# Kernel tuning notes

Measured on AMD Instinct MI355X. Metric: run time of the kernel, lower is better.

## Reference

```python
import jax, jax.numpy as jnp
import numpy as np

OUT_F, IN_F, RANK = 4096, 4096, 32
N_TOK = 8192  # batch 4 * seq 2048, flattened


def setup_inputs() -> dict:
    key = jax.random.key(0)
    k_x, k_w, k_s, k_a, k_b, k_bias = jax.random.split(key, 6)
    x = jax.random.normal(k_x, (N_TOK, IN_F), dtype=jnp.float32)
    # ternary weights in {-1, 0, +1}, stored as int8 buffer
    weight_q = (jax.random.randint(k_w, (OUT_F, IN_F), 0, 3) - 1).astype(jnp.int8)
    # per-output-channel absmean scale, shape [out, 1], positive
    scale = 0.02 + 0.05 * jax.random.uniform(k_s, (OUT_F, 1), dtype=jnp.float32)
    lora_A = 0.01 * jax.random.normal(k_a, (OUT_F, RANK), dtype=jnp.float32)
    lora_B = 0.01 * jax.random.normal(k_b, (RANK, IN_F), dtype=jnp.float32)
    bias = 0.01 * jax.random.normal(k_bias, (OUT_F,), dtype=jnp.float32)
    return {"x": x, "weight_q": weight_q, "scale": scale,
            "lora_A": lora_A, "lora_B": lora_B, "bias": bias}


def reference(x, weight_q, scale, lora_A, lora_B, bias):
    # out = (x @ W_q^T) * scale_per_out_channel + x @ B^T @ A^T + bias
    Wq = weight_q.astype(x.dtype)                       # dequantize {-1,0,1}
    out = jnp.einsum('ti,oi->to', x, Wq) * scale.reshape(1, -1)
    # low-rank LoRA residual: (x @ B^T) @ A^T, rank-RANK bottleneck
    out = out + (x @ lora_B.T) @ lora_A.T
    out = out + bias
    return out
```

## Files before the change

### kernel.cpp

```cpp
#include <hip/hip_runtime.h>
#include <stdint.h>

typedef unsigned short u16;
typedef __attribute__((ext_vector_type(8))) __bf16 bf16x8;
typedef __attribute__((ext_vector_type(4))) float f32x4;

__device__ __forceinline__ u16 f2bf(float f) {
  unsigned int u = __builtin_bit_cast(unsigned int, f);
  u = (u + 0x7FFFu + ((u >> 16) & 1u)) >> 16;
  return (u16)u;
}
__device__ __forceinline__ u16 tern2bf(int s) {
  return s == 0 ? (u16)0 : (s > 0 ? (u16)0x3F80 : (u16)0xBF80);
}

#define GLOAD_LDS16(g, l)                                                          \
  __builtin_amdgcn_global_load_lds((__attribute__((address_space(1))) void*)(g),   \
                                   (__attribute__((address_space(3))) void*)(l),   \
                                   16, 0, 0)

#define M_TOK 8192
#define N_OUT 4096
#define K_IN  4096
#define RANK  32

#define WS_XB    0ull
#define WS_WB    67108864ull
#define WS_BB    100663296ull
#define WS_A32   100925440ull
#define WS_T32   101187584ull
#define WS_TPART 101711872ull
#define WS_FLAG  110100480ull

__global__ void k_convert_x(const float4* __restrict__ x, ushort4* __restrict__ xb, int n4) {
  int stride = gridDim.x * blockDim.x;
  for (int i = blockIdx.x * blockDim.x + threadIdx.x; i < n4; i += stride) {
    float4 v = x[i];
    ushort4 o;
    o.x = f2bf(v.x); o.y = f2bf(v.y); o.z = f2bf(v.z); o.w = f2bf(v.w);
    xb[i] = o;
  }
}

__global__ void k_detect_wtype(const int* __restrict__ w, int* __restrict__ flag) {
  int v = w[threadIdx.x];
  bool ok = (v >= -1 && v <= 1);
  unsigned long long m = __ballot(ok);
  if (threadIdx.x == 0) *flag = (m == ~0ull) ? 1 : 0;
}

__global__ void k_convert_w(const void* __restrict__ wq, const int* __restrict__ flag,
                            ushort4* __restrict__ wb, int n4) {
  int is32 = *flag;
  int stride = gridDim.x * blockDim.x;
  for (int i = blockIdx.x * blockDim.x + threadIdx.x; i < n4; i += stride) {
    int s0, s1, s2, s3;
    if (is32) {
      int4 c = ((const int4*)wq)[i];
      s0 = c.x; s1 = c.y; s2 = c.z; s3 = c.w;
    } else {
      char4 c = ((const char4*)wq)[i];
      s0 = c.x; s1 = c.y; s2 = c.z; s3 = c.w;
    }
    ushort4 o;
    o.x = tern2bf(s0); o.y = tern2bf(s1); o.z = tern2bf(s2); o.w = tern2bf(s3);
    wb[i] = o;
  }
}

__global__ void k_prep_B(const float* __restrict__ loraB, u16* __restrict__ bb) {
  int idx = blockIdx.x * blockDim.x + threadIdx.x;
  if (idx < RANK * K_IN) bb[idx] = f2bf(loraB[idx]);
}

__global__ void k_prep_A(const float* __restrict__ loraA, const float* __restrict__ scale,
                         u16* __restrict__ a32) {
  int idx = blockIdx.x * blockDim.x + threadIdx.x;
  if (idx >= N_OUT * RANK) return;
  int o = idx >> 5;
  a32[idx] = f2bf(loraA[idx] / scale[o]);
}

__global__ __launch_bounds__(256) void k_lora_T(const u16* __restrict__ xb,
                                                const u16* __restrict__ bb,
                                                float* __restrict__ tpart) {
  __shared__ u16 As[64 * 32];
  __shared__ u16 Bs[32 * 32];
  int mt = blockIdx.x >> 3;
  int ks = blockIdx.x & 7;
  int tid = threadIdx.x, lane = tid & 63, wv = tid >> 6;
  int m0 = mt * 64;
  int kbase0 = ks * 512;
  f32x4 acc[2] = {};
  for (int step = 0; step < 16; ++step) {
    int kb = kbase0 + step * 32;
    __syncthreads();
    {
      const u16* src = xb + (size_t)(m0 + (tid >> 2)) * K_IN + kb + (tid & 3) * 8;
      GLOAD_LDS16(src, &As[tid * 8]);
    }
    if (tid < 128) {
      const u16* src = bb + (size_t)(tid >> 2) * K_IN + kb + (tid & 3) * 8;
      GLOAD_LDS16(src, &Bs[tid * 8]);
    }
    __syncthreads();
    bf16x8 a = *(const bf16x8*)&As[(wv * 16 + (lane & 15)) * 32 + (lane >> 4) * 8];
#pragma unroll
    for (int ni = 0; ni < 2; ++ni) {
      bf16x8 b = *(const bf16x8*)&Bs[(ni * 16 + (lane & 15)) * 32 + (lane >> 4) * 8];
      acc[ni] = __builtin_amdgcn_mfma_f32_16x16x32_bf16(a, b, acc[ni], 0, 0, 0);
    }
  }
#pragma unroll
  for (int ni = 0; ni < 2; ++ni)
#pragma unroll
    for (int r = 0; r < 4; ++r) {
      int row = m0 + wv * 16 + (lane >> 4) * 4 + r;
      int col = ni * 16 + (lane & 15);
      tpart[((size_t)ks * M_TOK + row) * RANK + col] = acc[ni][r];
    }
}

__global__ void k_reduce_T(const float* __restrict__ tpart, u16* __restrict__ t32) {
  int idx = blockIdx.x * blockDim.x + threadIdx.x;
  if (idx >= M_TOK * RANK) return;
  int t = idx >> 5, r = idx & 31;
  float v = 0.f;
#pragma unroll
  for (int s = 0; s < 8; ++s) v += tpart[((size_t)s * M_TOK + t) * RANK + r];
  t32[idx] = f2bf(v);
}

__global__ __launch_bounds__(1024, 4) void k_gemm8(const u16* __restrict__ xb,
                                                   const u16* __restrict__ wb,
                                                   const u16* __restrict__ t32,
                                                   const u16* __restrict__ a32,
                                                   const float* __restrict__ scale,
                                                   const float* __restrict__ bias,
                                                   float* __restrict__ out) {
  __shared__ u16 As[4][8192];
  __shared__ u16 Bs[4][8192];
  const int tid = threadIdx.x;
  const int l = tid & 63, w = tid >> 6;
  const int wm = w >> 2, wn = w & 3;
  const int bid = blockIdx.x;
  const int swz = (bid & 7) * 64 + (bid >> 3);
  const int m0 = (swz >> 4) * 256, n0 = (swz & 15) * 256;

  const int srow = tid >> 2;
  const int scx = ((tid & 3) ^ ((tid >> 3) & 3)) * 8;
  const int ldst = tid * 8;
  const int r15 = l & 15;
  const int cxr = (((l >> 4) ^ ((r15 >> 1) & 3)) * 8);

  f32x4 acc[4][4] = {};

  u16* AsF = &As[0][0];
  u16* BsF = &Bs[0][0];
  const u16* axs = xb + (size_t)(m0 + srow) * K_IN + scx;
  const u16* bxs = wb + (size_t)(n0 + srow) * K_IN + scx;

#pragma unroll
  for (int ts = 0; ts < 3; ++ts) {
    GLOAD_LDS16(axs + ts * 32, AsF + ts * 8192 + ldst);
    GLOAD_LDS16(bxs + ts * 32, BsF + ts * 8192 + ldst);
  }
  asm volatile("s_waitcnt vmcnt(4)" ::: "memory");
  asm volatile("s_barrier" ::: "memory");

  const int abase = (wm * 64 + r15) * 32 + cxr;
  const int bbase = (wn * 64 + r15) * 32 + cxr;

  const u16* ap = axs + 96;
  const u16* bp = bxs + 96;

  bf16x8 fa[4], fb[4];

#define SA(DST) { GLOAD_LDS16(ap, AsF + (DST) * 8192 + ldst); ap += 32; }
#define SB(DST) { GLOAD_LDS16(bp, BsF + (DST) * 8192 + ldst); bp += 32; }
#define W2  asm volatile("s_waitcnt vmcnt(2)" ::: "memory");
#define W0  asm volatile("s_waitcnt vmcnt(0)" ::: "memory");
#define BARR asm volatile("s_barrier" ::: "memory");
#define READN(NS)                                                                   \
  { const u16* An = AsF + (NS) * 8192;                                              \
    const u16* Bn = BsF + (NS) * 8192;                                              \
    _Pragma("unroll") for (int mi = 0; mi < 4; ++mi)                                \
        fa[mi] = *(const bf16x8*)&An[abase + mi * 512];                             \
    _Pragma("unroll") for (int nj = 0; nj < 4; ++nj)                                \
        fb[nj] = *(const bf16x8*)&Bn[bbase + nj * 512]; }

#define TILE(STAGE, WAIT, RD, BAR)                                                  \
  {                                                                                 \
    STAGE                                                                           \
    __builtin_amdgcn_s_setprio(1);                                                  \
    _Pragma("unroll") for (int mi = 0; mi < 4; ++mi)                                \
    _Pragma("unroll") for (int nj = 0; nj < 4; ++nj)                                \
        acc[mi][nj] =                                                               \
            __builtin_amdgcn_mfma_f32_16x16x32_bf16(fa[mi], fb[nj], acc[mi][nj], 0, 0, 0); \
    __builtin_amdgcn_s_setprio(0);                                                  \
    WAIT                                                                            \
    RD                                                                              \
    BAR                                                                             \
  }

  READN(0)

#pragma unroll 1
  for (int t = 0; t < 124; t += 4) {
    TILE(SA(3) SB(3), W2, READN(1), BARR)
    TILE(SA(0) SB(0), W2, READN(2), BARR)
    TILE(SA(1) SB(1), W2, READN(3), BARR)
    TILE(SA(2) SB(2), W2, READN(0), BARR)
  }
  TILE(SA(3) SB(3), W2, READN(1), BARR)
  {
    const u16* la = t32 + (size_t)(m0 + srow) * RANK + scx;
    const u16* lb = a32 + (size_t)(n0 + srow) * RANK + scx;
    TILE({ GLOAD_LDS16(la, AsF + 0 * 8192 + ldst); GLOAD_LDS16(lb, BsF + 0 * 8192 + ldst); },
         W2, READN(2), BARR)
  }
  TILE(, W0, READN(3), BARR)
  TILE(, , READN(0), BARR)
  TILE(, , , )

#pragma unroll
  for (int nj = 0; nj < 4; ++nj) {
    int col = n0 + wn * 64 + nj * 16 + r15;
    float s = scale[col], bv = bias[col];
#pragma unroll
    for (int mi = 0; mi < 4; ++mi) {
      int row = m0 + wm * 64 + mi * 16 + (l >> 4) * 4;
#pragma unroll
      for (int r = 0; r < 4; ++r)
        out[(size_t)(row + r) * N_OUT + col] = acc[mi][nj][r] * s + bv;
    }
  }
}

extern "C" void kernel_launch(void* const* d_in, const int* in_sizes, int n_in,
                              void* d_out, int out_size, void* d_ws, size_t ws_size,
                              hipStream_t stream) {
  const float* x     = (const float*)d_in[0];
  const void*  wq    = d_in[1];
  const float* scale = (const float*)d_in[2];
  const float* loraA = (const float*)d_in[3];
  const float* loraB = (const float*)d_in[4];
  const float* bias  = (const float*)d_in[5];
  float* out = (float*)d_out;

  char* ws = (char*)d_ws;
  u16*   xb    = (u16*)(ws + WS_XB);
  u16*   wbuf  = (u16*)(ws + WS_WB);
  u16*   bb    = (u16*)(ws + WS_BB);
  u16*   a32   = (u16*)(ws + WS_A32);
  u16*   t32   = (u16*)(ws + WS_T32);
  float* tpart = (float*)(ws + WS_TPART);
  int*   flag  = (int*)(ws + WS_FLAG);

  k_convert_x<<<2048, 256, 0, stream>>>((const float4*)x, (ushort4*)xb, M_TOK * K_IN / 4);
  k_detect_wtype<<<1, 64, 0, stream>>>((const int*)wq, flag);
  k_prep_B<<<512, 256, 0, stream>>>(loraB, bb);
  k_prep_A<<<512, 256, 0, stream>>>(loraA, scale, a32);
  k_convert_w<<<2048, 256, 0, stream>>>(wq, flag, (ushort4*)wbuf, N_OUT * K_IN / 4);
  k_lora_T<<<1024, 256, 0, stream>>>(xb, bb, tpart);
  k_reduce_T<<<1024, 256, 0, stream>>>(tpart, t32);
  k_gemm8<<<512, 1024, 0, stream>>>(xb, wbuf, t32, a32, scale, bias, out);

  (void)in_sizes; (void)n_in; (void)out_size; (void)ws_size;
}
```

Measured before the change: 315.5 us.

## Keep ternary weights as int8 in GEMM and expand to bf16 in registers

```diff
diff --git a/kernel.cpp b/kernel.cpp
--- a/kernel.cpp
+++ b/kernel.cpp
@@ -10,8 +10,17 @@
   u = (u + 0x7FFFu + ((u >> 16) & 1u)) >> 16;
   return (u16)u;
 }
-__device__ __forceinline__ u16 tern2bf(int s) {
-  return s == 0 ? (u16)0 : (s > 0 ? (u16)0x3F80 : (u16)0xBF80);
+__device__ __forceinline__ bf16x8 expand8(unsigned q0, unsigned q1) {
+  unsigned x = (q0 & 0xFFu) | ((q0 & 0xFF00u) << 8);
+  unsigned y = ((q0 >> 16) & 0xFFu) | ((q0 >> 8) & 0xFF0000u);
+  unsigned z = (q1 & 0xFFu) | ((q1 & 0xFF00u) << 8);
+  unsigned w = ((q1 >> 16) & 0xFFu) | ((q1 >> 8) & 0xFF0000u);
+  uint4 o;
+  o.x = ((x & 0x10001u) * 0x3F80u) | ((x & 0x800080u) << 8);
+  o.y = ((y & 0x10001u) * 0x3F80u) | ((y & 0x800080u) << 8);
+  o.z = ((z & 0x10001u) * 0x3F80u) | ((z & 0x800080u) << 8);
+  o.w = ((w & 0x10001u) * 0x3F80u) | ((w & 0x800080u) << 8);
+  return __builtin_bit_cast(bf16x8, o);
 }
 
 #define GLOAD_LDS16(g, l)                                                          \
@@ -49,22 +58,29 @@
   if (threadIdx.x == 0) *flag = (m == ~0ull) ? 1 : 0;
 }
 
-__global__ void k_convert_w(const void* __restrict__ wq, const int* __restrict__ flag,
-                            ushort4* __restrict__ wb, int n4) {
+__global__ void k_convert_w8(const void* __restrict__ wq, const int* __restrict__ flag,
+                             char* __restrict__ wb8) {
   int is32 = *flag;
   int stride = gridDim.x * blockDim.x;
-  for (int i = blockIdx.x * blockDim.x + threadIdx.x; i < n4; i += stride) {
-    int s0, s1, s2, s3;
+  int total = N_OUT * K_IN / 8;
+  for (int i = blockIdx.x * blockDim.x + threadIdx.x; i < total; i += stride) {
+    int row = i >> 9;
+    int jb = (i & 511) * 8;
+    uint2 pk;
     if (is32) {
-      int4 c = ((const int4*)wq)[i];
-      s0 = c.x; s1 = c.y; s2 = c.z; s3 = c.w;
+      const int* s = (const int*)wq + (size_t)row * K_IN + jb;
+      unsigned lo = 0, hi = 0;
+#pragma unroll
+      for (int k2 = 0; k2 < 4; ++k2) lo |= ((unsigned)s[k2] & 0xFFu) << (8 * k2);
+#pragma unroll
+      for (int k2 = 0; k2 < 4; ++k2) hi |= ((unsigned)s[4 + k2] & 0xFFu) << (8 * k2);
+      pk.x = lo; pk.y = hi;
     } else {
-      char4 c = ((const char4*)wq)[i];
-      s0 = c.x; s1 = c.y; s2 = c.z; s3 = c.w;
-    }
-    ushort4 o;
-    o.x = tern2bf(s0); o.y = tern2bf(s1); o.z = tern2bf(s2); o.w = tern2bf(s3);
-    wb[i] = o;
+      pk = *(const uint2*)((const char*)wq + (size_t)row * K_IN + jb);
+    }
+    int jin = jb & 63, g = jb >> 6;
+    int p = ((jin >> 3) & 3) * 16 + (jin >> 5) * 8;
+    *(uint2*)(wb8 + (size_t)row * K_IN + (g << 6) + p) = pk;
   }
 }
 
@@ -132,14 +148,14 @@
 }
 
 __global__ __launch_bounds__(1024, 4) void k_gemm8(const u16* __restrict__ xb,
-                                                   const u16* __restrict__ wb,
+                                                   const char* __restrict__ wb8,
                                                    const u16* __restrict__ t32,
                                                    const u16* __restrict__ a32,
                                                    const float* __restrict__ scale,
                                                    const float* __restrict__ bias,
                                                    float* __restrict__ out) {
   __shared__ u16 As[4][8192];
-  __shared__ u16 Bs[4][8192];
+  __shared__ char Bs8[4][16384];
   const int tid = threadIdx.x;
   const int l = tid & 63, w = tid >> 6;
   const int wm = w >> 2, wn = w & 3;
@@ -152,44 +168,64 @@
   const int ldst = tid * 8;
   const int r15 = l & 15;
   const int cxr = (((l >> 4) ^ ((r15 >> 1) & 3)) * 8);
+  const int cxB = (((l >> 4) ^ ((r15 >> 1) & 3)) * 16);
 
   f32x4 acc[4][4] = {};
 
   u16* AsF = &As[0][0];
-  u16* BsF = &Bs[0][0];
+  char* Bs8F = &Bs8[0][0];
   const u16* axs = xb + (size_t)(m0 + srow) * K_IN + scx;
-  const u16* bxs = wb + (size_t)(n0 + srow) * K_IN + scx;
-
-#pragma unroll
-  for (int ts = 0; ts < 3; ++ts) {
-    GLOAD_LDS16(axs + ts * 32, AsF + ts * 8192 + ldst);
-    GLOAD_LDS16(bxs + ts * 32, BsF + ts * 8192 + ldst);
-  }
-  asm volatile("s_waitcnt vmcnt(4)" ::: "memory");
+  const char* bsrc = wb8 + (size_t)(n0 + (tid >> 2)) * 4096 +
+                     (size_t)(((tid & 3) ^ ((tid >> 3) & 3)) * 16);
+
+  GLOAD_LDS16(bsrc, Bs8F + 0 * 16384 + tid * 16); bsrc += 64;
+  GLOAD_LDS16(bsrc, Bs8F + 1 * 16384 + tid * 16); bsrc += 64;
+#pragma unroll
+  for (int ts = 0; ts < 3; ++ts) GLOAD_LDS16(axs + ts * 32, AsF + ts * 8192 + ldst);
+  asm volatile("s_waitcnt vmcnt(1)" ::: "memory");
   asm volatile("s_barrier" ::: "memory");
 
   const int abase = (wm * 64 + r15) * 32 + cxr;
-  const int bbase = (wn * 64 + r15) * 32 + cxr;
+  const int bb8base = (wn * 64 + r15) * 64 + cxB;
+  const int lbbase = (wn * 64 + r15) * 32 + cxr;
 
   const u16* ap = axs + 96;
-  const u16* bp = bxs + 96;
 
   bf16x8 fa[4], fb[4];
+  uint2 stash[4];
 
 #define SA(DST) { GLOAD_LDS16(ap, AsF + (DST) * 8192 + ldst); ap += 32; }
-#define SB(DST) { GLOAD_LDS16(bp, BsF + (DST) * 8192 + ldst); bp += 32; }
+#define SBP(DST) { GLOAD_LDS16(bsrc, Bs8F + (DST) * 16384 + tid * 16); bsrc += 64; }
+#define SLB { GLOAD_LDS16(a32 + (size_t)(n0 + srow) * RANK + scx, Bs8F + 16384 + ldst * 2); }
+#define SAL { GLOAD_LDS16(t32 + (size_t)(m0 + srow) * RANK + scx, AsF + 0 * 8192 + ldst); }
 #define W2  asm volatile("s_waitcnt vmcnt(2)" ::: "memory");
+#define W1  asm volatile("s_waitcnt vmcnt(1)" ::: "memory");
 #define W0  asm volatile("s_waitcnt vmcnt(0)" ::: "memory");
 #define BARR asm volatile("s_barrier" ::: "memory");
-#define READN(NS)                                                                   \
+#define RDE(NS, BS)                                                                 \
   { const u16* An = AsF + (NS) * 8192;                                              \
-    const u16* Bn = BsF + (NS) * 8192;                                              \
+    _Pragma("unroll") for (int mi = 0; mi < 4; ++mi)                                \
+        fa[mi] = *(const bf16x8*)&An[abase + mi * 512];                             \
+    const char* Bn = Bs8F + (BS) * 16384;                                           \
+    _Pragma("unroll") for (int nj = 0; nj < 4; ++nj) {                              \
+      uint4 r_ = *(const uint4*)&Bn[bb8base + nj * 1024];                           \
+      fb[nj] = expand8(r_.x, r_.y);                                                 \
+      stash[nj] = make_uint2(r_.z, r_.w); } }
+#define RDO(NS)                                                                     \
+  { const u16* An = AsF + (NS) * 8192;                                              \
     _Pragma("unroll") for (int mi = 0; mi < 4; ++mi)                                \
         fa[mi] = *(const bf16x8*)&An[abase + mi * 512];                             \
     _Pragma("unroll") for (int nj = 0; nj < 4; ++nj)                                \
-        fb[nj] = *(const bf16x8*)&Bn[bbase + nj * 512]; }
-
-#define TILE(STAGE, WAIT, RD, BAR)                                                  \
+        fb[nj] = expand8(stash[nj].x, stash[nj].y); }
+#define RDL                                                                         \
+  { const u16* An = AsF;                                                            \
+    _Pragma("unroll") for (int mi = 0; mi < 4; ++mi)                                \
+        fa[mi] = *(const bf16x8*)&An[abase + mi * 512];                             \
+    const u16* Ln = (const u16*)(Bs8F + 16384);                                     \
+    _Pragma("unroll") for (int nj = 0; nj < 4; ++nj)                                \
+        fb[nj] = *(const bf16x8*)&Ln[lbbase + nj * 512]; }
+
+#define TILE(STAGE, WAIT, RD)                                                       \
   {                                                                                 \
     STAGE                                                                           \
     __builtin_amdgcn_s_setprio(1);                                                  \
@@ -200,28 +236,31 @@
     __builtin_amdgcn_s_setprio(0);                                                  \
     WAIT                                                                            \
     RD                                                                              \
-    BAR                                                                             \
-  }
-
-  READN(0)
+    BARR                                                                            \
+  }
+
+  RDE(0, 0)
 
 #pragma unroll 1
-  for (int t = 0; t < 124; t += 4) {
-    TILE(SA(3) SB(3), W2, READN(1), BARR)
-    TILE(SA(0) SB(0), W2, READN(2), BARR)
-    TILE(SA(1) SB(1), W2, READN(3), BARR)
-    TILE(SA(2) SB(2), W2, READN(0), BARR)
-  }
-  TILE(SA(3) SB(3), W2, READN(1), BARR)
-  {
-    const u16* la = t32 + (size_t)(m0 + srow) * RANK + scx;
-    const u16* lb = a32 + (size_t)(n0 + srow) * RANK + scx;
-    TILE({ GLOAD_LDS16(la, AsF + 0 * 8192 + ldst); GLOAD_LDS16(lb, BsF + 0 * 8192 + ldst); },
-         W2, READN(2), BARR)
-  }
-  TILE(, W0, READN(3), BARR)
-  TILE(, , READN(0), BARR)
-  TILE(, , , )
+  for (int it = 0; it < 15; ++it) {
+    TILE(SA(3) SBP(2), W2, RDO(1))
+    TILE(SA(0),        W1, RDE(2, 1))
+    TILE(SA(1) SBP(3), W2, RDO(3))
+    TILE(SA(2),        W1, RDE(0, 2))
+    TILE(SA(3) SBP(0), W2, RDO(1))
+    TILE(SA(0),        W1, RDE(2, 3))
+    TILE(SA(1) SBP(1), W2, RDO(3))
+    TILE(SA(2),        W1, RDE(0, 0))
+  }
+  TILE(SA(3) SBP(2), W2, RDO(1))
+  TILE(SA(0),        W1, RDE(2, 1))
+  TILE(SA(1) SBP(3), W2, RDO(3))
+  TILE(SA(2),        W1, RDE(0, 2))
+  TILE(SA(3) SLB,    W2, RDO(1))
+  TILE(SAL,          W2, RDE(2, 3))
+  TILE(,             W0, RDO(3))
+  TILE(,             ,   RDL)
+  TILE(,             ,   )
 
 #pragma unroll
   for (int nj = 0; nj < 4; ++nj) {
@@ -250,7 +289,7 @@
 
   char* ws = (char*)d_ws;
   u16*   xb    = (u16*)(ws + WS_XB);
-  u16*   wbuf  = (u16*)(ws + WS_WB);
+  char*  wb8   = (char*)(ws + WS_WB);
   u16*   bb    = (u16*)(ws + WS_BB);
   u16*   a32   = (u16*)(ws + WS_A32);
   u16*   t32   = (u16*)(ws + WS_T32);
@@ -261,10 +300,10 @@
   k_detect_wtype<<<1, 64, 0, stream>>>((const int*)wq, flag);
   k_prep_B<<<512, 256, 0, stream>>>(loraB, bb);
   k_prep_A<<<512, 256, 0, stream>>>(loraA, scale, a32);
-  k_convert_w<<<2048, 256, 0, stream>>>(wq, flag, (ushort4*)wbuf, N_OUT * K_IN / 4);
+  k_convert_w8<<<2048, 256, 0, stream>>>(wq, flag, wb8);
   k_lora_T<<<1024, 256, 0, stream>>>(xb, bb, tpart);
   k_reduce_T<<<1024, 256, 0, stream>>>(tpart, t32);
-  k_gemm8<<<512, 1024, 0, stream>>>(xb, wbuf, t32, a32, scale, bias, out);
+  k_gemm8<<<512, 1024, 0, stream>>>(xb, wb8, t32, a32, scale, bias, out);
 
   (void)in_sizes; (void)n_in; (void)out_size; (void)ws_size;
 }
```

New measurement: 468.6 us. 48.5% more time.
